# Optimization experiments

Measured on AMD Instinct MI355X. Metric: run time of the kernel, lower is better.

Reference implementation:

```python
import jax, jax.numpy as jnp
import numpy as np

B, CIN, N, K, G, COUT = 8, 128, 2048, 16, 4, 256
NL = COUT // 4          # nl_channels = int(0.25*out_channels) = 64
L = COUT - NL           # l_channels = 192
CL = L // G             # 48 per local head
CNL = NL // G           # 16 per non-local head


def setup_inputs() -> dict:
    key = jax.random.key(0)
    ks = jax.random.split(key, 16)
    s = 0.05
    r = lambda k_, sh: s * jax.random.normal(k_, sh, jnp.float32)
    return {
        "x": jax.random.normal(ks[0], (B, CIN, N, K), jnp.float32),
        "abs_x": jax.random.normal(ks[1], (B, CIN // 2, N, 1), jnp.float32),
        "points": jax.random.normal(ks[2], (B, 3, N), jnp.float32),
        "Wq": r(ks[3], (L, CIN // 2)),
        "Wk": r(ks[4], (L, CIN // 2)),
        "Wv": r(ks[5], (L, CIN)),
        "Wnq": r(ks[6], (NL, CIN // 2)),
        "Wnk": r(ks[7], (NL, CIN // 2)),
        "Wnv1": r(ks[8], (NL, CIN // 2)),
        "Wnv2": r(ks[9], (NL, CIN // 2)),
        "pe_w1": r(ks[10], (3, L)),
        "pe_b1": jnp.zeros((L,), jnp.float32),
        "pe_w2": r(ks[11], (L, L)),
        "pe_b2": jnp.zeros((L,), jnp.float32),
        "npe_w1": r(ks[12], (G, 3, CNL)),
        "npe_b1": jnp.zeros((G, CNL), jnp.float32),
        "npe_w2": r(ks[13], (G, CNL, CNL)),
        "npe_b2": jnp.zeros((G, CNL), jnp.float32),
        "idx": jax.random.randint(ks[14], (B, 1, N, K), 0, N, dtype=jnp.int32),
    }


def _forward(x, abs_x, points, Wq, Wk, Wv, Wnq, Wnk, Wnv1, Wnv2,
             pe_w1, pe_b1, pe_w2, pe_b2, npe_w1, npe_b1, npe_w2, npe_b2, idx):
    b, c, n, k = x.shape
    half = c // 2
    idx_sq = idx[:, 0]                                   # (b,n,k)

    # ---- 1. Local attention over kNN neighbors ----
    lq = jnp.einsum('oc,bcns->bons', Wq, abs_x).reshape(b, G, CL, n, 1)
    lk = jnp.einsum('oc,bcnk->bonk', Wk, x[:, half:] + x[:, :half]).reshape(b, G, CL, n, k)
    lv = jnp.einsum('oc,bcnk->bonk', Wv, x).reshape(b, G, CL, n, k)

    # absolute positional encoding (select_neighbors -> carte MLP)
    nbr = jax.vmap(lambda p, i: p[:, i])(points, idx_sq)  # (b,3,n,k)
    rel = nbr - nbr[..., 0:1]                             # subtract first neighbor
    h = jax.nn.relu(jnp.einsum('bcnk,cd->bnkd', rel, pe_w1) + pe_b1)
    pe = (jnp.einsum('bnkd,de->bnke', h, pe_w2) + pe_b2).transpose(0, 3, 1, 2)
    lk = lk + pe.reshape(b, G, CL, n, k)

    att = jax.nn.softmax((lq * lk).sum(2), axis=-1)       # (b,G,n,k)
    local_feature = jnp.einsum('bgnk,bgcnk->bgcn', att, lv).reshape(b, L, n, 1)

    # ---- scatter-based sparse attention centrality + top-k node selection ----
    idx_flat = idx_sq.reshape(b, n * k)
    att_flat = att.reshape(b, G, n * k)

    def scat(a_g, i):  # a_g: (G, n*k), i: (n*k,)
        return jax.vmap(lambda a: jnp.zeros((n,), a.dtype).at[i].add(a))(a_g)

    cent = jax.vmap(scat)(att_flat, idx_flat)             # (b,G,n)
    vals, inds = jax.lax.top_k(cent, k)                   # (b,G,k)

    # ---- 2. Non-local MHA over selected nodes ----
    a2 = abs_x[..., 0]                                    # (b,half,n)
    nq = jnp.einsum('oc,bcn->bon', Wnq, a2).reshape(b, G, CNL, n)
    nk_ = jnp.einsum('oc,bcn->bon', Wnk, a2).reshape(b, G, CNL, n)
    nv1 = jnp.einsum('oc,bcn->bon', Wnv1, a2).reshape(b, G, CNL, n)
    nv2 = jnp.einsum('oc,bcn->bon', Wnv2, a2).reshape(b, G, CNL, n)

    gi = inds[:, :, None, :]                              # (b,G,1,k)
    nk_sel = jnp.take_along_axis(nk_, gi, axis=3)         # (b,G,CNL,k)
    nv2j = jnp.take_along_axis(nv2, gi, axis=3)           # (b,G,CNL,k)

    # per-group non-local positional encoding (constant over n by construction)
    sel = jnp.take_along_axis(jnp.broadcast_to(points[:, None], (b, G, 3, n)), gi, axis=3)  # (b,G,3,k)
    rel_nl = sel - sel[..., 0:1]
    h2 = jax.nn.relu(jnp.einsum('bgck,gcd->bgkd', rel_nl, npe_w1) + npe_b1[None, :, None, :])
    pe_nl = (jnp.einsum('bgkd,gde->bgke', h2, npe_w2) + npe_b2[None, :, None, :]).transpose(0, 1, 3, 2)  # (b,G,CNL,k)

    att_nl = jax.nn.softmax(jnp.einsum('bgcn,bgck->bgnk', nq, nk_sel + pe_nl), axis=-1)
    # value[b,g,c,n,k] = nv1[...,n] - nv2[...,n] + nv2j[...,k], gated by tanh(centrality)
    w = att_nl * jnp.tanh(vals)[:, :, None, :]            # (b,G,n,k)
    s = w.sum(-1)                                         # (b,G,n)
    nl_feature = (nv1 - nv2) * s[:, :, None, :] + jnp.einsum('bgnk,bgck->bgcn', w, nv2j)
    nl_feature = nl_feature.reshape(b, NL, n, 1)

    return jnp.concatenate([local_feature, nl_feature], axis=1)  # (b,COUT,n,1)


def reference(x, abs_x, points, Wq, Wk, Wv, Wnq, Wnk, Wnv1, Wnv2,
              pe_w1, pe_b1, pe_w2, pe_b2, npe_w1, npe_b1, npe_w2, npe_b2, idx):
    return _forward(x, abs_x, points, Wq, Wk, Wv, Wnq, Wnk, Wnv1, Wnv2,
                    pe_w1, pe_b1, pe_w2, pe_b2, npe_w1, npe_b1, npe_w2, npe_b2, idx)
```

## Files before the change

kernel.cpp:

```cpp
#include <hip/hip_runtime.h>
#include <cstddef>

constexpr int NN = 2048;
constexpr int GG = 4;

__global__ __launch_bounds__(256) void prep_q(const float* __restrict__ Wq,
                                              const float* __restrict__ Wk,
                                              const float* __restrict__ pe_w2,
                                              float* __restrict__ Qbuf) {
    const int g = blockIdx.x >> 6, c2 = blockIdx.x & 63;
    const int row = threadIdx.x;
    float acc = 0.f;
    if (row < 64) {
        for (int j = 0; j < 48; ++j) {
            const int o = g * 48 + j;
            acc = fmaf(Wk[o * 64 + row], Wq[o * 64 + c2], acc);
        }
    } else {
        const int d = row - 64;
        for (int j = 0; j < 48; ++j) {
            const int o = g * 48 + j;
            acc = fmaf(pe_w2[(size_t)d * 192 + o], Wq[o * 64 + c2], acc);
        }
    }
    Qbuf[((size_t)(g * 64 + c2) << 8) + row] = acc;
}

__global__ __launch_bounds__(256, 3) void local_v4(
    const float* __restrict__ x, const float* __restrict__ abs_x,
    const float* __restrict__ points, const float* __restrict__ Wv,
    const float* __restrict__ pe_w1, const float* __restrict__ pe_b1,
    const int* __restrict__ idx, const float* __restrict__ Qbuf,
    float* __restrict__ out, float* __restrict__ cent)
{
    const int bn = blockIdx.x;
    const int b  = bn >> 8;
    const int n0 = (bn & 255) << 3;
    const int tid = threadIdx.x;

    __shared__ int   sidx[128];
    __shared__ float sa2[64][8];
    __shared__ float spts[3][8][16];
    __shared__ float sq[4][8][65];
    __shared__ __align__(16) float s_union[4 * 8 * 193];
    __shared__ float spartA[128][9];
    __shared__ float spartB[128][9];
    __shared__ float satt[4][128];

    float* sw  = s_union;
    float* sxw = s_union;

    if (tid < 128) sidx[tid] = idx[((size_t)b * NN + n0) * 16 + tid];
    for (int i = tid; i < 512; i += 256) {
        int c = i >> 3, nl = i & 7;
        sa2[c][nl] = abs_x[((size_t)b * 64 + c) * NN + n0 + nl];
    }
    __syncthreads();

    for (int i = tid; i < 384; i += 256) {
        int c = i >> 7, r = i & 127;
        spts[c][r >> 4][r & 15] = points[((size_t)b * 3 + c) * NN + sidx[r]];
    }
    for (int g = 0; g < 4; ++g) {
        const float* qb = Qbuf + ((size_t)g << 14) + tid;
        float acc[8] = {0.f, 0.f, 0.f, 0.f, 0.f, 0.f, 0.f, 0.f};
        for (int c2 = 0; c2 < 64; ++c2) {
            const float qv = qb[c2 << 8];
            const float4 a0 = *(const float4*)&sa2[c2][0];
            const float4 a1 = *(const float4*)&sa2[c2][4];
            acc[0] = fmaf(qv, a0.x, acc[0]); acc[1] = fmaf(qv, a0.y, acc[1]);
            acc[2] = fmaf(qv, a0.z, acc[2]); acc[3] = fmaf(qv, a0.w, acc[3]);
            acc[4] = fmaf(qv, a1.x, acc[4]); acc[5] = fmaf(qv, a1.y, acc[5]);
            acc[6] = fmaf(qv, a1.z, acc[6]); acc[7] = fmaf(qv, a1.w, acc[7]);
        }
        if (tid < 64) {
            #pragma unroll
            for (int nl = 0; nl < 8; ++nl) sq[g][nl][tid] = acc[nl];
        } else {
            #pragma unroll
            for (int nl = 0; nl < 8; ++nl) sw[((g << 3) + nl) * 193 + (tid - 64)] = acc[nl];
        }
    }
    __syncthreads();

    {
        const int col = tid & 127, ch = tid >> 7;
        const int nl = col >> 4, kk = col & 15;
        const float* xp = x + (((size_t)(b * 128 + ch * 32) * NN) + n0 + nl) * 16 + kk;
        const float* q0 = &sq[0][nl][ch * 32];
        const float* q1 = &sq[1][nl][ch * 32];
        const float* q2 = &sq[2][nl][ch * 32];
        const float* q3 = &sq[3][nl][ch * 32];
        float a0 = 0.f, a1 = 0.f, a2 = 0.f, a3 = 0.f;
        for (int i = 0; i < 32; ++i) {
            const float xs = xp[0] + xp[(size_t)64 * NN * 16];
            xp += NN * 16;
            a0 = fmaf(q0[i], xs, a0);
            a1 = fmaf(q1[i], xs, a1);
            a2 = fmaf(q2[i], xs, a2);
            a3 = fmaf(q3[i], xs, a3);
        }
        spartA[col][ch * 4 + 0] = a0; spartA[col][ch * 4 + 1] = a1;
        spartA[col][ch * 4 + 2] = a2; spartA[col][ch * 4 + 3] = a3;
    }
    {
        const int col = tid & 127, dh = tid >> 7;
        const int nl = col >> 4, kk = col & 15;
        const float r0 = spts[0][nl][kk] - spts[0][nl][0];
        const float r1 = spts[1][nl][kk] - spts[1][nl][0];
        const float r2 = spts[2][nl][kk] - spts[2][nl][0];
        float p0 = 0.f, p1 = 0.f, p2 = 0.f, p3 = 0.f;
        const int d0 = dh * 96;
        const float* w0 = &sw[((0 << 3) + nl) * 193];
        const float* w1 = &sw[((1 << 3) + nl) * 193];
        const float* w2 = &sw[((2 << 3) + nl) * 193];
        const float* w3 = &sw[((3 << 3) + nl) * 193];
        for (int d = d0; d < d0 + 96; ++d) {
            float h = fmaf(r0, pe_w1[d], fmaf(r1, pe_w1[192 + d], fmaf(r2, pe_w1[384 + d], pe_b1[d])));
            h = fmaxf(h, 0.f);
            p0 = fmaf(h, w0[d], p0);
            p1 = fmaf(h, w1[d], p1);
            p2 = fmaf(h, w2[d], p2);
            p3 = fmaf(h, w3[d], p3);
        }
        spartB[col][dh * 4 + 0] = p0; spartB[col][dh * 4 + 1] = p1;
        spartB[col][dh * 4 + 2] = p2; spartB[col][dh * 4 + 3] = p3;
    }
    __syncthreads();

    if (tid < 32) {
        const int g = tid >> 3, nl = tid & 7;
        float lg[16], m = -1e30f;
        #pragma unroll
        for (int kk = 0; kk < 16; ++kk) {
            const int col = nl * 16 + kk;
            lg[kk] = (spartA[col][g] + spartA[col][4 + g])
                   + (spartB[col][g] + spartB[col][4 + g]);
            m = fmaxf(m, lg[kk]);
        }
        float s = 0.f;
        #pragma unroll
        for (int kk = 0; kk < 16; ++kk) { lg[kk] = __expf(lg[kk] - m); s += lg[kk]; }
        const float inv = 1.f / s;
        #pragma unroll
        for (int kk = 0; kk < 16; ++kk) {
            const float a = lg[kk] * inv;
            satt[g][nl * 16 + kk] = a;
            atomicAdd(&cent[((size_t)(b * GG + g) << 11) + sidx[nl * 16 + kk]], a);
        }
    }
    __syncthreads();

    #pragma unroll
    for (int t = 0; t < 4; ++t) {
        const int i2 = t * 256 + tid;
        const int c = i2 >> 3, nl = i2 & 7;
        const float* xp = x + (((size_t)(b * 128 + c) * NN) + n0 + nl) * 16;
        const float4 x0 = *(const float4*)(xp);
        const float4 x1 = *(const float4*)(xp + 4);
        const float4 x2 = *(const float4*)(xp + 8);
        const float4 x3 = *(const float4*)(xp + 12);
        const float xv[16] = {x0.x, x0.y, x0.z, x0.w, x1.x, x1.y, x1.z, x1.w,
                              x2.x, x2.y, x2.z, x2.w, x3.x, x3.y, x3.z, x3.w};
        #pragma unroll
        for (int g = 0; g < 4; ++g) {
            float v = 0.f;
            #pragma unroll
            for (int kk = 0; kk < 16; ++kk) v = fmaf(xv[kk], satt[g][nl * 16 + kk], v);
            sxw[((g << 7) + c) * 8 + nl] = v;
        }
    }
    __syncthreads();

    for (int i = tid; i < 1536; i += 256) {
        const int o = i >> 3, nl = i & 7;
        const int g = o / 48;
        const float* wv = Wv + (size_t)o * 128;
        const float* xwp = &sxw[(size_t)(g << 7) * 8 + nl];
        float a = 0.f;
        for (int c = 0; c < 128; c += 4) {
            const float4 w4 = *(const float4*)(wv + c);
            a = fmaf(w4.x, xwp[(c + 0) * 8], a);
            a = fmaf(w4.y, xwp[(c + 1) * 8], a);
            a = fmaf(w4.z, xwp[(c + 2) * 8], a);
            a = fmaf(w4.w, xwp[(c + 3) * 8], a);
        }
        out[(((size_t)b << 8) + o) * NN + n0 + nl] = a;
    }
}

__global__ __launch_bounds__(256) void topk_prep_kernel(
    const float* __restrict__ abs_x, const float* __restrict__ points,
    const float* __restrict__ Wnk, const float* __restrict__ Wnv2,
    const float* __restrict__ npe_w1, const float* __restrict__ npe_b1,
    const float* __restrict__ npe_w2, const float* __restrict__ npe_b2,
    const float* __restrict__ cent,
    float* __restrict__ nkpe, float* __restrict__ nv2j, float* __restrict__ tanhv)
{
    const int bg  = blockIdx.x;
    const int b   = bg >> 2, g = bg & 3;
    const int tid = threadIdx.x;
    __shared__ float sc[2048];
    __shared__ float rv[4];  __shared__ int ri[4];
    __shared__ float svals[16]; __shared__ int sinds[16];
    __shared__ float srel[3][16];
    __shared__ float sh2[16][16];

    for (int i = tid; i < 2048; i += 256) sc[i] = cent[((size_t)bg << 11) + i];
    __syncthreads();
    for (int t = 0; t < 16; ++t) {
        float bv = -1e30f; int bi = 1 << 30;
        for (int i = tid; i < 2048; i += 256) {
            float v = sc[i];
            if (v > bv) { bv = v; bi = i; }
        }
        #pragma unroll
        for (int off = 1; off < 64; off <<= 1) {
            float ov = __shfl_xor(bv, off, 64);
            int   oi = __shfl_xor(bi, off, 64);
            if (ov > bv || (ov == bv && oi < bi)) { bv = ov; bi = oi; }
        }
        if ((tid & 63) == 0) { rv[tid >> 6] = bv; ri[tid >> 6] = bi; }
        __syncthreads();
        if (tid == 0) {
            for (int w = 1; w < 4; ++w)
                if (rv[w] > bv || (rv[w] == bv && ri[w] < bi)) { bv = rv[w]; bi = ri[w]; }
            svals[t] = bv; sinds[t] = bi;
            sc[bi] = -1e30f;
        }
        __syncthreads();
    }

    if (tid < 48) {
        int c = tid >> 4, j = tid & 15;
        srel[c][j] = points[((size_t)b * 3 + c) * NN + sinds[j]]
                   - points[((size_t)b * 3 + c) * NN + sinds[0]];
    }
    __syncthreads();
    {
        int j = tid >> 4, d = tid & 15;
        float a = npe_b1[g * 16 + d];
        #pragma unroll
        for (int c = 0; c < 3; ++c) a = fmaf(srel[c][j], npe_w1[((g * 3 + c) << 4) + d], a);
        sh2[j][d] = fmaxf(a, 0.f);
    }
    __syncthreads();
    {
        int c = tid >> 4, j = tid & 15;
        float a = npe_b2[g * 16 + c];
        #pragma unroll
        for (int d = 0; d < 16; ++d) a = fmaf(sh2[j][d], npe_w2[((g * 16 + d) << 4) + c], a);
        float nk = 0.f, nv = 0.f;
        const int col = sinds[j];
        const float* a2  = abs_x + (size_t)b * 64 * NN + col;
        const float* wkr = Wnk  + ((size_t)(g * 16 + c) << 6);
        const float* wvr = Wnv2 + ((size_t)(g * 16 + c) << 6);
        for (int ci = 0; ci < 64; ++ci) {
            float av = a2[(size_t)ci * NN];
            nk = fmaf(wkr[ci], av, nk);
            nv = fmaf(wvr[ci], av, nv);
        }
        nkpe[((size_t)bg << 8) + (c << 4) + j] = nk + a;
        nv2j[((size_t)bg << 8) + (c << 4) + j] = nv;
    }
    if (tid < 16) tanhv[(bg << 4) + tid] = tanhf(svals[tid]);
}

__global__ __launch_bounds__(256) void nonlocal_kernel(
    const float* __restrict__ abs_x,
    const float* __restrict__ Wnq, const float* __restrict__ Wnv1, const float* __restrict__ Wnv2,
    const float* __restrict__ nkpe, const float* __restrict__ nv2j, const float* __restrict__ tanhv,
    float* __restrict__ out)
{
    const int blk = blockIdx.x;
    const int b   = blk >> 5;
    const int n0  = (blk & 31) << 6;
    const int tid = threadIdx.x;
    const int nl  = tid & 63;
    const int g   = tid >> 6;

    __shared__ float sa2[64][64];
    __shared__ float snkpe[4][16][16];
    __shared__ float snv2j[4][16][16];
    __shared__ float stanh[4][16];

    for (int i = tid; i < 64 * 64; i += 256) {
        int ci = i >> 6, c2 = i & 63;
        sa2[ci][c2] = abs_x[((size_t)b * 64 + ci) * NN + n0 + c2];
    }
    for (int i = tid; i < 1024; i += 256) {
        ((float*)snkpe)[i] = nkpe[((size_t)b << 10) + i];
        ((float*)snv2j)[i] = nv2j[((size_t)b << 10) + i];
    }
    if (tid < 64) ((float*)stanh)[tid] = tanhv[(b << 6) + tid];
    __syncthreads();

    float nq[16], nv1[16], nv2[16];
    #pragma unroll
    for (int c = 0; c < 16; ++c) { nq[c] = 0.f; nv1[c] = 0.f; nv2[c] = 0.f; }
    const float* wq  = Wnq  + (size_t)(g << 4) * 64;
    const float* wv1 = Wnv1 + (size_t)(g << 4) * 64;
    const float* wv2 = Wnv2 + (size_t)(g << 4) * 64;
    for (int ci = 0; ci < 64; ++ci) {
        const float a = sa2[ci][nl];
        #pragma unroll
        for (int c = 0; c < 16; ++c) {
            nq[c]  = fmaf(wq [(c << 6) + ci], a, nq[c]);
            nv1[c] = fmaf(wv1[(c << 6) + ci], a, nv1[c]);
            nv2[c] = fmaf(wv2[(c << 6) + ci], a, nv2[c]);
        }
    }

    float lg[16];
    #pragma unroll
    for (int j = 0; j < 16; ++j) {
        float a = 0.f;
        #pragma unroll
        for (int c = 0; c < 16; ++c) a = fmaf(nq[c], snkpe[g][c][j], a);
        lg[j] = a;
    }
    float m = lg[0];
    #pragma unroll
    for (int j = 1; j < 16; ++j) m = fmaxf(m, lg[j]);
    float s = 0.f;
    float w[16];
    #pragma unroll
    for (int j = 0; j < 16; ++j) { w[j] = __expf(lg[j] - m); s += w[j]; }
    const float inv = 1.f / s;
    float ws = 0.f;
    #pragma unroll
    for (int j = 0; j < 16; ++j) { w[j] = w[j] * inv * stanh[g][j]; ws += w[j]; }
    #pragma unroll
    for (int c = 0; c < 16; ++c) {
        float v = (nv1[c] - nv2[c]) * ws;
        #pragma unroll
        for (int j = 0; j < 16; ++j) v = fmaf(w[j], snv2j[g][c][j], v);
        out[(((size_t)b << 8) + 192 + (g << 4) + c) * NN + n0 + nl] = v;
    }
}

extern "C" void kernel_launch(void* const* d_in, const int* in_sizes, int n_in,
                              void* d_out, int out_size, void* d_ws, size_t ws_size,
                              hipStream_t stream)
{
    (void)in_sizes; (void)n_in; (void)out_size; (void)ws_size;
    const float* x      = (const float*)d_in[0];
    const float* abs_x  = (const float*)d_in[1];
    const float* points = (const float*)d_in[2];
    const float* Wq     = (const float*)d_in[3];
    const float* Wk     = (const float*)d_in[4];
    const float* Wv     = (const float*)d_in[5];
    const float* Wnq    = (const float*)d_in[6];
    const float* Wnk    = (const float*)d_in[7];
    const float* Wnv1   = (const float*)d_in[8];
    const float* Wnv2   = (const float*)d_in[9];
    const float* pe_w1  = (const float*)d_in[10];
    const float* pe_b1  = (const float*)d_in[11];
    const float* pe_w2  = (const float*)d_in[12];
    const float* npe_w1 = (const float*)d_in[14];
    const float* npe_b1 = (const float*)d_in[15];
    const float* npe_w2 = (const float*)d_in[16];
    const float* npe_b2 = (const float*)d_in[17];
    const int*   idx    = (const int*)d_in[18];
    float* out = (float*)d_out;

    float* cent  = (float*)d_ws;
    float* Qbuf  = cent + 65536;
    float* nkpeW = Qbuf + 65536;
    float* nv2jW = nkpeW + 8192;
    float* tanhW = nv2jW + 8192;

    hipMemsetAsync(cent, 0, (size_t)65536 * sizeof(float), stream);
    prep_q<<<256, 256, 0, stream>>>(Wq, Wk, pe_w2, Qbuf);
    local_v4<<<2048, 256, 0, stream>>>(x, abs_x, points, Wv, pe_w1, pe_b1,
                                       idx, Qbuf, out, cent);
    topk_prep_kernel<<<32, 256, 0, stream>>>(abs_x, points, Wnk, Wnv2,
                                             npe_w1, npe_b1, npe_w2, npe_b2,
                                             cent, nkpeW, nv2jW, tanhW);
    nonlocal_kernel<<<8 * 32, 256, 0, stream>>>(abs_x, Wnq, Wnv1, Wnv2,
                                                nkpeW, nv2jW, tanhW, out);
}
```

Baseline: 235.0 us.

## Halve points per block in local kernel and prefetch x before softmax

The local attention kernel now handles 4 points per block instead of 8. That doubles the grid to 4096 blocks, shrinks shared memory, and raises the launch-bounds occupancy hint from 3 to 4 blocks. The logit reductions are split four ways across channel and d ranges instead of two. The x tile used in the weighted sum is loaded into registers before the softmax so its latency overlaps the softmax phase. Costs include recomputing Q/W projections per block twice as often, more register pressure from holding 32 prefetched values, and less reuse of Wv loads per block.

```diff
diff --git a/kernel.cpp b/kernel.cpp
--- a/kernel.cpp
+++ b/kernel.cpp
@@ -26,7 +26,7 @@
     Qbuf[((size_t)(g * 64 + c2) << 8) + row] = acc;
 }
 
-__global__ __launch_bounds__(256, 3) void local_v4(
+__global__ __launch_bounds__(256, 4) void local_v5(
     const float* __restrict__ x, const float* __restrict__ abs_x,
     const float* __restrict__ points, const float* __restrict__ Wv,
     const float* __restrict__ pe_w1, const float* __restrict__ pe_b1,
@@ -34,88 +34,90 @@
     float* __restrict__ out, float* __restrict__ cent)
 {
     const int bn = blockIdx.x;
-    const int b  = bn >> 8;
-    const int n0 = (bn & 255) << 3;
+    const int b  = bn >> 9;
+    const int n0 = (bn & 511) << 2;
     const int tid = threadIdx.x;
 
-    __shared__ int   sidx[128];
-    __shared__ float sa2[64][8];
-    __shared__ float spts[3][8][16];
-    __shared__ float sq[4][8][65];
-    __shared__ __align__(16) float s_union[4 * 8 * 193];
-    __shared__ float spartA[128][9];
-    __shared__ float spartB[128][9];
-    __shared__ float satt[4][128];
+    __shared__ int   sidx[64];
+    __shared__ float sa2[64][4];
+    __shared__ float spts[3][4][16];
+    __shared__ float sq[4][4][65];
+    __shared__ __align__(16) float s_union[3104];
+    __shared__ float spartA[64][17];
+    __shared__ float spartB[64][17];
+    __shared__ float satt[4][64];
 
     float* sw  = s_union;
     float* sxw = s_union;
 
-    if (tid < 128) sidx[tid] = idx[((size_t)b * NN + n0) * 16 + tid];
-    for (int i = tid; i < 512; i += 256) {
-        int c = i >> 3, nl = i & 7;
+    if (tid < 64) sidx[tid] = idx[((size_t)b * NN + n0) * 16 + tid];
+    if (tid < 256) {
+        int c = tid >> 2, nl = tid & 3;
         sa2[c][nl] = abs_x[((size_t)b * 64 + c) * NN + n0 + nl];
     }
     __syncthreads();
 
-    for (int i = tid; i < 384; i += 256) {
-        int c = i >> 7, r = i & 127;
+    if (tid < 192) {
+        int c = tid >> 6, r = tid & 63;
         spts[c][r >> 4][r & 15] = points[((size_t)b * 3 + c) * NN + sidx[r]];
     }
+    #pragma unroll
     for (int g = 0; g < 4; ++g) {
         const float* qb = Qbuf + ((size_t)g << 14) + tid;
-        float acc[8] = {0.f, 0.f, 0.f, 0.f, 0.f, 0.f, 0.f, 0.f};
+        float a0 = 0.f, a1 = 0.f, a2v = 0.f, a3 = 0.f;
         for (int c2 = 0; c2 < 64; ++c2) {
             const float qv = qb[c2 << 8];
-            const float4 a0 = *(const float4*)&sa2[c2][0];
-            const float4 a1 = *(const float4*)&sa2[c2][4];
-            acc[0] = fmaf(qv, a0.x, acc[0]); acc[1] = fmaf(qv, a0.y, acc[1]);
-            acc[2] = fmaf(qv, a0.z, acc[2]); acc[3] = fmaf(qv, a0.w, acc[3]);
-            acc[4] = fmaf(qv, a1.x, acc[4]); acc[5] = fmaf(qv, a1.y, acc[5]);
-            acc[6] = fmaf(qv, a1.z, acc[6]); acc[7] = fmaf(qv, a1.w, acc[7]);
+            const float4 av = *(const float4*)&sa2[c2][0];
+            a0 = fmaf(qv, av.x, a0); a1 = fmaf(qv, av.y, a1);
+            a2v = fmaf(qv, av.z, a2v); a3 = fmaf(qv, av.w, a3);
         }
         if (tid < 64) {
-            #pragma unroll
-            for (int nl = 0; nl < 8; ++nl) sq[g][nl][tid] = acc[nl];
+            sq[g][0][tid] = a0; sq[g][1][tid] = a1;
+            sq[g][2][tid] = a2v; sq[g][3][tid] = a3;
         } else {
-            #pragma unroll
-            for (int nl = 0; nl < 8; ++nl) sw[((g << 3) + nl) * 193 + (tid - 64)] = acc[nl];
+            const int d = tid - 64;
+            sw[((g << 2) + 0) * 193 + d] = a0;
+            sw[((g << 2) + 1) * 193 + d] = a1;
+            sw[((g << 2) + 2) * 193 + d] = a2v;
+            sw[((g << 2) + 3) * 193 + d] = a3;
         }
     }
     __syncthreads();
 
     {
-        const int col = tid & 127, ch = tid >> 7;
+        const int col = tid & 63, ch = tid >> 6;
         const int nl = col >> 4, kk = col & 15;
-        const float* xp = x + (((size_t)(b * 128 + ch * 32) * NN) + n0 + nl) * 16 + kk;
-        const float* q0 = &sq[0][nl][ch * 32];
-        const float* q1 = &sq[1][nl][ch * 32];
-        const float* q2 = &sq[2][nl][ch * 32];
-        const float* q3 = &sq[3][nl][ch * 32];
-        float a0 = 0.f, a1 = 0.f, a2 = 0.f, a3 = 0.f;
-        for (int i = 0; i < 32; ++i) {
+        const float* xp = x + (((size_t)(b * 128 + ch * 16) * NN) + n0 + nl) * 16 + kk;
+        const float* q0 = &sq[0][nl][ch * 16];
+        const float* q1 = &sq[1][nl][ch * 16];
+        const float* q2 = &sq[2][nl][ch * 16];
+        const float* q3 = &sq[3][nl][ch * 16];
+        float a0 = 0.f, a1 = 0.f, a2v = 0.f, a3 = 0.f;
+        #pragma unroll 4
+        for (int i = 0; i < 16; ++i) {
             const float xs = xp[0] + xp[(size_t)64 * NN * 16];
             xp += NN * 16;
             a0 = fmaf(q0[i], xs, a0);
             a1 = fmaf(q1[i], xs, a1);
-            a2 = fmaf(q2[i], xs, a2);
+            a2v = fmaf(q2[i], xs, a2v);
             a3 = fmaf(q3[i], xs, a3);
         }
         spartA[col][ch * 4 + 0] = a0; spartA[col][ch * 4 + 1] = a1;
-        spartA[col][ch * 4 + 2] = a2; spartA[col][ch * 4 + 3] = a3;
+        spartA[col][ch * 4 + 2] = a2v; spartA[col][ch * 4 + 3] = a3;
     }
     {
-        const int col = tid & 127, dh = tid >> 7;
+        const int col = tid & 63, dh = tid >> 6;
         const int nl = col >> 4, kk = col & 15;
         const float r0 = spts[0][nl][kk] - spts[0][nl][0];
         const float r1 = spts[1][nl][kk] - spts[1][nl][0];
         const float r2 = spts[2][nl][kk] - spts[2][nl][0];
         float p0 = 0.f, p1 = 0.f, p2 = 0.f, p3 = 0.f;
-        const int d0 = dh * 96;
-        const float* w0 = &sw[((0 << 3) + nl) * 193];
-        const float* w1 = &sw[((1 << 3) + nl) * 193];
-        const float* w2 = &sw[((2 << 3) + nl) * 193];
-        const float* w3 = &sw[((3 << 3) + nl) * 193];
-        for (int d = d0; d < d0 + 96; ++d) {
+        const int d0 = dh * 48;
+        const float* w0 = &sw[((0 << 2) + nl) * 193];
+        const float* w1 = &sw[((1 << 2) + nl) * 193];
+        const float* w2 = &sw[((2 << 2) + nl) * 193];
+        const float* w3 = &sw[((3 << 2) + nl) * 193];
+        for (int d = d0; d < d0 + 48; ++d) {
             float h = fmaf(r0, pe_w1[d], fmaf(r1, pe_w1[192 + d], fmaf(r2, pe_w1[384 + d], pe_b1[d])));
             h = fmaxf(h, 0.f);
             p0 = fmaf(h, w0[d], p0);
@@ -128,14 +130,26 @@
     }
     __syncthreads();
 
-    if (tid < 32) {
-        const int g = tid >> 3, nl = tid & 7;
+    float xv[2][16];
+    #pragma unroll
+    for (int t = 0; t < 2; ++t) {
+        const int i2 = t * 256 + tid;
+        const int c = i2 >> 2, nl = i2 & 3;
+        const float* xp = x + (((size_t)(b * 128 + c) * NN) + n0 + nl) * 16;
+        *(float4*)&xv[t][0]  = *(const float4*)(xp);
+        *(float4*)&xv[t][4]  = *(const float4*)(xp + 4);
+        *(float4*)&xv[t][8]  = *(const float4*)(xp + 8);
+        *(float4*)&xv[t][12] = *(const float4*)(xp + 12);
+    }
+
+    if (tid < 16) {
+        const int g = tid >> 2, nl = tid & 3;
         float lg[16], m = -1e30f;
         #pragma unroll
         for (int kk = 0; kk < 16; ++kk) {
             const int col = nl * 16 + kk;
-            lg[kk] = (spartA[col][g] + spartA[col][4 + g])
-                   + (spartB[col][g] + spartB[col][4 + g]);
+            lg[kk] = (spartA[col][g] + spartA[col][4 + g] + spartA[col][8 + g] + spartA[col][12 + g])
+                   + (spartB[col][g] + spartB[col][4 + g] + spartB[col][8 + g] + spartB[col][12 + g]);
             m = fmaxf(m, lg[kk]);
         }
         float s = 0.f;
@@ -152,38 +166,33 @@
     __syncthreads();
 
     #pragma unroll
-    for (int t = 0; t < 4; ++t) {
+    for (int t = 0; t < 2; ++t) {
         const int i2 = t * 256 + tid;
-        const int c = i2 >> 3, nl = i2 & 7;
-        const float* xp = x + (((size_t)(b * 128 + c) * NN) + n0 + nl) * 16;
-        const float4 x0 = *(const float4*)(xp);
-        const float4 x1 = *(const float4*)(xp + 4);
-        const float4 x2 = *(const float4*)(xp + 8);
-        const float4 x3 = *(const float4*)(xp + 12);
-        const float xv[16] = {x0.x, x0.y, x0.z, x0.w, x1.x, x1.y, x1.z, x1.w,
-                              x2.x, x2.y, x2.z, x2.w, x3.x, x3.y, x3.z, x3.w};
+        const int c = i2 >> 2, nl = i2 & 3;
         #pragma unroll
         for (int g = 0; g < 4; ++g) {
             float v = 0.f;
             #pragma unroll
-            for (int kk = 0; kk < 16; ++kk) v = fmaf(xv[kk], satt[g][nl * 16 + kk], v);
-            sxw[((g << 7) + c) * 8 + nl] = v;
-        }
-    }
-    __syncthreads();
-
-    for (int i = tid; i < 1536; i += 256) {
-        const int o = i >> 3, nl = i & 7;
+            for (int kk = 0; kk < 16; ++kk) v = fmaf(xv[t][kk], satt[g][nl * 16 + kk], v);
+            sxw[(((g << 7) + c) << 2) + nl] = v;
+        }
+    }
+    __syncthreads();
+
+    #pragma unroll
+    for (int rep = 0; rep < 3; ++rep) {
+        const int i = rep * 256 + tid;
+        const int o = i >> 2, nl = i & 3;
         const int g = o / 48;
         const float* wv = Wv + (size_t)o * 128;
-        const float* xwp = &sxw[(size_t)(g << 7) * 8 + nl];
+        const float* xwp = &sxw[((size_t)(g << 7) << 2) + nl];
         float a = 0.f;
         for (int c = 0; c < 128; c += 4) {
             const float4 w4 = *(const float4*)(wv + c);
-            a = fmaf(w4.x, xwp[(c + 0) * 8], a);
-            a = fmaf(w4.y, xwp[(c + 1) * 8], a);
-            a = fmaf(w4.z, xwp[(c + 2) * 8], a);
-            a = fmaf(w4.w, xwp[(c + 3) * 8], a);
+            a = fmaf(w4.x, xwp[(c + 0) << 2], a);
+            a = fmaf(w4.y, xwp[(c + 1) << 2], a);
+            a = fmaf(w4.z, xwp[(c + 2) << 2], a);
+            a = fmaf(w4.w, xwp[(c + 3) << 2], a);
         }
         out[(((size_t)b << 8) + o) * NN + n0 + nl] = a;
     }
@@ -372,7 +381,7 @@
 
     hipMemsetAsync(cent, 0, (size_t)65536 * sizeof(float), stream);
     prep_q<<<256, 256, 0, stream>>>(Wq, Wk, pe_w2, Qbuf);
-    local_v4<<<2048, 256, 0, stream>>>(x, abs_x, points, Wv, pe_w1, pe_b1,
+    local_v5<<<4096, 256, 0, stream>>>(x, abs_x, points, Wv, pe_w1, pe_b1,
                                        idx, Qbuf, out, cent);
     topk_prep_kernel<<<32, 256, 0, stream>>>(abs_x, points, Wnk, Wnv2,
                                              npe_w1, npe_b1, npe_w2, npe_b2,
```

After: 248.6 us. +5.8%, slower.

## Shrink local kernel shared memory and raise occupancy; widen topk block

Applied to the files above, without the earlier changes.

Restructures the local attention kernel to cut shared memory: the q-projection and positional-weight buffers now share one aliased region, the positional-encoding weights are computed two groups at a time in two passes, and the two partial-logit arrays are merged into one accumulated array. Launch bounds rise from 3 to 6 blocks per CU. The Wv projection and attention-weighted sum switch to contiguous float4 shared reads, and the centrality atomics move to the end of the kernel. The topk kernel now uses 512 threads per block. The extra passes add barriers and recompute work, traded for more resident waves to hide global load latency.

```diff
diff --git a/kernel.cpp b/kernel.cpp
--- a/kernel.cpp
+++ b/kernel.cpp
@@ -26,7 +26,7 @@
     Qbuf[((size_t)(g * 64 + c2) << 8) + row] = acc;
 }
 
-__global__ __launch_bounds__(256, 3) void local_v4(
+__global__ __launch_bounds__(256, 6) void local_v7(
     const float* __restrict__ x, const float* __restrict__ abs_x,
     const float* __restrict__ points, const float* __restrict__ Wv,
     const float* __restrict__ pe_w1, const float* __restrict__ pe_b1,
@@ -40,15 +40,15 @@
 
     __shared__ int   sidx[128];
     __shared__ float sa2[64][8];
-    __shared__ float spts[3][8][16];
-    __shared__ float sq[4][8][65];
-    __shared__ __align__(16) float s_union[4 * 8 * 193];
-    __shared__ float spartA[128][9];
-    __shared__ float spartB[128][9];
-    __shared__ float satt[4][128];
-
-    float* sw  = s_union;
-    float* sxw = s_union;
+    __shared__ __align__(16) float s_big[4224];
+    __shared__ float spart[128][9];
+    __shared__ float s_small[544];
+
+    float* sq   = s_big;
+    float* sw2  = s_big;
+    float* sxw  = s_big;
+    float* spts = s_small;
+    float* satt = s_small;
 
     if (tid < 128) sidx[tid] = idx[((size_t)b * NN + n0) * 16 + tid];
     for (int i = tid; i < 512; i += 256) {
@@ -58,84 +58,122 @@
     __syncthreads();
 
     for (int i = tid; i < 384; i += 256) {
-        int c = i >> 7, r = i & 127;
-        spts[c][r >> 4][r & 15] = points[((size_t)b * 3 + c) * NN + sidx[r]];
-    }
-    for (int g = 0; g < 4; ++g) {
-        const float* qb = Qbuf + ((size_t)g << 14) + tid;
-        float acc[8] = {0.f, 0.f, 0.f, 0.f, 0.f, 0.f, 0.f, 0.f};
+        int c3 = i >> 7, r = i & 127;
+        spts[(c3 * 8 + (r >> 4)) * 16 + (r & 15)] =
+            points[((size_t)b * 3 + c3) * NN + sidx[r]];
+    }
+    {
+        const int g = tid >> 6, row = tid & 63;
+        const float* qb = Qbuf + (((size_t)g * 64) << 8) + row;
+        float a0 = 0.f, a1 = 0.f, a2v = 0.f, a3 = 0.f,
+              a4 = 0.f, a5 = 0.f, a6 = 0.f, a7 = 0.f;
         for (int c2 = 0; c2 < 64; ++c2) {
             const float qv = qb[c2 << 8];
-            const float4 a0 = *(const float4*)&sa2[c2][0];
-            const float4 a1 = *(const float4*)&sa2[c2][4];
-            acc[0] = fmaf(qv, a0.x, acc[0]); acc[1] = fmaf(qv, a0.y, acc[1]);
-            acc[2] = fmaf(qv, a0.z, acc[2]); acc[3] = fmaf(qv, a0.w, acc[3]);
-            acc[4] = fmaf(qv, a1.x, acc[4]); acc[5] = fmaf(qv, a1.y, acc[5]);
-            acc[6] = fmaf(qv, a1.z, acc[6]); acc[7] = fmaf(qv, a1.w, acc[7]);
-        }
-        if (tid < 64) {
-            #pragma unroll
-            for (int nl = 0; nl < 8; ++nl) sq[g][nl][tid] = acc[nl];
-        } else {
-            #pragma unroll
-            for (int nl = 0; nl < 8; ++nl) sw[((g << 3) + nl) * 193 + (tid - 64)] = acc[nl];
-        }
-    }
-    __syncthreads();
+            const float4 v0 = *(const float4*)&sa2[c2][0];
+            const float4 v1 = *(const float4*)&sa2[c2][4];
+            a0 = fmaf(qv, v0.x, a0); a1 = fmaf(qv, v0.y, a1);
+            a2v = fmaf(qv, v0.z, a2v); a3 = fmaf(qv, v0.w, a3);
+            a4 = fmaf(qv, v1.x, a4); a5 = fmaf(qv, v1.y, a5);
+            a6 = fmaf(qv, v1.z, a6); a7 = fmaf(qv, v1.w, a7);
+        }
+        const int base = (g << 3) * 65 + row;
+        sq[base + 0 * 65] = a0; sq[base + 1 * 65] = a1;
+        sq[base + 2 * 65] = a2v; sq[base + 3 * 65] = a3;
+        sq[base + 4 * 65] = a4; sq[base + 5 * 65] = a5;
+        sq[base + 6 * 65] = a6; sq[base + 7 * 65] = a7;
+    }
+    __syncthreads();
+
+    const int col = tid & 127, dh = tid >> 7;
+    const int nlc = col >> 4, kkc = col & 15;
 
     {
-        const int col = tid & 127, ch = tid >> 7;
-        const int nl = col >> 4, kk = col & 15;
-        const float* xp = x + (((size_t)(b * 128 + ch * 32) * NN) + n0 + nl) * 16 + kk;
-        const float* q0 = &sq[0][nl][ch * 32];
-        const float* q1 = &sq[1][nl][ch * 32];
-        const float* q2 = &sq[2][nl][ch * 32];
-        const float* q3 = &sq[3][nl][ch * 32];
-        float a0 = 0.f, a1 = 0.f, a2 = 0.f, a3 = 0.f;
+        const float* xp = x + (((size_t)(b * 128 + dh * 32) * NN) + n0 + nlc) * 16 + kkc;
+        const float* q0 = &sq[((0 << 3) + nlc) * 65 + dh * 32];
+        const float* q1 = &sq[((1 << 3) + nlc) * 65 + dh * 32];
+        const float* q2 = &sq[((2 << 3) + nlc) * 65 + dh * 32];
+        const float* q3 = &sq[((3 << 3) + nlc) * 65 + dh * 32];
+        float a0 = 0.f, a1 = 0.f, a2v = 0.f, a3 = 0.f;
         for (int i = 0; i < 32; ++i) {
             const float xs = xp[0] + xp[(size_t)64 * NN * 16];
             xp += NN * 16;
             a0 = fmaf(q0[i], xs, a0);
             a1 = fmaf(q1[i], xs, a1);
-            a2 = fmaf(q2[i], xs, a2);
+            a2v = fmaf(q2[i], xs, a2v);
             a3 = fmaf(q3[i], xs, a3);
         }
-        spartA[col][ch * 4 + 0] = a0; spartA[col][ch * 4 + 1] = a1;
-        spartA[col][ch * 4 + 2] = a2; spartA[col][ch * 4 + 3] = a3;
-    }
-    {
-        const int col = tid & 127, dh = tid >> 7;
-        const int nl = col >> 4, kk = col & 15;
-        const float r0 = spts[0][nl][kk] - spts[0][nl][0];
-        const float r1 = spts[1][nl][kk] - spts[1][nl][0];
-        const float r2 = spts[2][nl][kk] - spts[2][nl][0];
-        float p0 = 0.f, p1 = 0.f, p2 = 0.f, p3 = 0.f;
-        const int d0 = dh * 96;
-        const float* w0 = &sw[((0 << 3) + nl) * 193];
-        const float* w1 = &sw[((1 << 3) + nl) * 193];
-        const float* w2 = &sw[((2 << 3) + nl) * 193];
-        const float* w3 = &sw[((3 << 3) + nl) * 193];
-        for (int d = d0; d < d0 + 96; ++d) {
-            float h = fmaf(r0, pe_w1[d], fmaf(r1, pe_w1[192 + d], fmaf(r2, pe_w1[384 + d], pe_b1[d])));
-            h = fmaxf(h, 0.f);
-            p0 = fmaf(h, w0[d], p0);
-            p1 = fmaf(h, w1[d], p1);
-            p2 = fmaf(h, w2[d], p2);
-            p3 = fmaf(h, w3[d], p3);
-        }
-        spartB[col][dh * 4 + 0] = p0; spartB[col][dh * 4 + 1] = p1;
-        spartB[col][dh * 4 + 2] = p2; spartB[col][dh * 4 + 3] = p3;
-    }
-    __syncthreads();
+        spart[col][dh * 4 + 0] = a0; spart[col][dh * 4 + 1] = a1;
+        spart[col][dh * 4 + 2] = a2v; spart[col][dh * 4 + 3] = a3;
+    }
+    __syncthreads();
+
+    const float r0 = spts[(0 * 8 + nlc) * 16 + kkc] - spts[(0 * 8 + nlc) * 16];
+    const float r1 = spts[(1 * 8 + nlc) * 16 + kkc] - spts[(1 * 8 + nlc) * 16];
+    const float r2 = spts[(2 * 8 + nlc) * 16 + kkc] - spts[(2 * 8 + nlc) * 16];
+    #pragma unroll
+    for (int p = 0; p < 2; ++p) {
+        if (tid < 192) {
+            const int d = tid;
+            float w00=0.f,w01=0.f,w02=0.f,w03=0.f,w04=0.f,w05=0.f,w06=0.f,w07=0.f;
+            float w10=0.f,w11=0.f,w12=0.f,w13=0.f,w14=0.f,w15=0.f,w16=0.f,w17=0.f;
+            const float* qb0 = Qbuf + (((size_t)(2 * p + 0) * 64) << 8) + 64 + d;
+            const float* qb1 = Qbuf + (((size_t)(2 * p + 1) * 64) << 8) + 64 + d;
+            for (int c2 = 0; c2 < 64; ++c2) {
+                const float qv0 = qb0[c2 << 8];
+                const float qv1 = qb1[c2 << 8];
+                const float4 v0 = *(const float4*)&sa2[c2][0];
+                const float4 v1 = *(const float4*)&sa2[c2][4];
+                w00 = fmaf(qv0, v0.x, w00); w01 = fmaf(qv0, v0.y, w01);
+                w02 = fmaf(qv0, v0.z, w02); w03 = fmaf(qv0, v0.w, w03);
+                w04 = fmaf(qv0, v1.x, w04); w05 = fmaf(qv0, v1.y, w05);
+                w06 = fmaf(qv0, v1.z, w06); w07 = fmaf(qv0, v1.w, w07);
+                w10 = fmaf(qv1, v0.x, w10); w11 = fmaf(qv1, v0.y, w11);
+                w12 = fmaf(qv1, v0.z, w12); w13 = fmaf(qv1, v0.w, w13);
+                w14 = fmaf(qv1, v1.x, w14); w15 = fmaf(qv1, v1.y, w15);
+                w16 = fmaf(qv1, v1.z, w16); w17 = fmaf(qv1, v1.w, w17);
+            }
+            sw2[(0 * 8 + 0) * 196 + d] = w00; sw2[(0 * 8 + 1) * 196 + d] = w01;
+            sw2[(0 * 8 + 2) * 196 + d] = w02; sw2[(0 * 8 + 3) * 196 + d] = w03;
+            sw2[(0 * 8 + 4) * 196 + d] = w04; sw2[(0 * 8 + 5) * 196 + d] = w05;
+            sw2[(0 * 8 + 6) * 196 + d] = w06; sw2[(0 * 8 + 7) * 196 + d] = w07;
+            sw2[(1 * 8 + 0) * 196 + d] = w10; sw2[(1 * 8 + 1) * 196 + d] = w11;
+            sw2[(1 * 8 + 2) * 196 + d] = w12; sw2[(1 * 8 + 3) * 196 + d] = w13;
+            sw2[(1 * 8 + 4) * 196 + d] = w14; sw2[(1 * 8 + 5) * 196 + d] = w15;
+            sw2[(1 * 8 + 6) * 196 + d] = w16; sw2[(1 * 8 + 7) * 196 + d] = w17;
+        }
+        __syncthreads();
+        {
+            float pB0 = 0.f, pB1 = 0.f;
+            const float* w0 = &sw2[(0 * 8 + nlc) * 196];
+            const float* w1 = &sw2[(1 * 8 + nlc) * 196];
+            const int d0 = dh * 96;
+            for (int d = d0; d < d0 + 96; d += 4) {
+                const float4 w1a = *(const float4*)&pe_w1[d];
+                const float4 w1b = *(const float4*)&pe_w1[192 + d];
+                const float4 w1c = *(const float4*)&pe_w1[384 + d];
+                const float4 bb  = *(const float4*)&pe_b1[d];
+                const float h0 = fmaxf(fmaf(r0, w1a.x, fmaf(r1, w1b.x, fmaf(r2, w1c.x, bb.x))), 0.f);
+                const float h1 = fmaxf(fmaf(r0, w1a.y, fmaf(r1, w1b.y, fmaf(r2, w1c.y, bb.y))), 0.f);
+                const float h2 = fmaxf(fmaf(r0, w1a.z, fmaf(r1, w1b.z, fmaf(r2, w1c.z, bb.z))), 0.f);
+                const float h3 = fmaxf(fmaf(r0, w1a.w, fmaf(r1, w1b.w, fmaf(r2, w1c.w, bb.w))), 0.f);
+                const float4 wa = *(const float4*)&w0[d];
+                const float4 wb = *(const float4*)&w1[d];
+                pB0 = fmaf(h0, wa.x, fmaf(h1, wa.y, fmaf(h2, wa.z, fmaf(h3, wa.w, pB0))));
+                pB1 = fmaf(h0, wb.x, fmaf(h1, wb.y, fmaf(h2, wb.z, fmaf(h3, wb.w, pB1))));
+            }
+            spart[col][dh * 4 + 2 * p + 0] += pB0;
+            spart[col][dh * 4 + 2 * p + 1] += pB1;
+        }
+        __syncthreads();
+    }
 
     if (tid < 32) {
         const int g = tid >> 3, nl = tid & 7;
         float lg[16], m = -1e30f;
         #pragma unroll
         for (int kk = 0; kk < 16; ++kk) {
-            const int col = nl * 16 + kk;
-            lg[kk] = (spartA[col][g] + spartA[col][4 + g])
-                   + (spartB[col][g] + spartB[col][4 + g]);
+            const int cc = nl * 16 + kk;
+            lg[kk] = spart[cc][g] + spart[cc][4 + g];
             m = fmaxf(m, lg[kk]);
         }
         float s = 0.f;
@@ -143,11 +181,7 @@
         for (int kk = 0; kk < 16; ++kk) { lg[kk] = __expf(lg[kk] - m); s += lg[kk]; }
         const float inv = 1.f / s;
         #pragma unroll
-        for (int kk = 0; kk < 16; ++kk) {
-            const float a = lg[kk] * inv;
-            satt[g][nl * 16 + kk] = a;
-            atomicAdd(&cent[((size_t)(b * GG + g) << 11) + sidx[nl * 16 + kk]], a);
-        }
+        for (int kk = 0; kk < 16; ++kk) satt[nl * 68 + g * 16 + kk] = lg[kk] * inv;
     }
     __syncthreads();
 
@@ -160,36 +194,50 @@
         const float4 x1 = *(const float4*)(xp + 4);
         const float4 x2 = *(const float4*)(xp + 8);
         const float4 x3 = *(const float4*)(xp + 12);
-        const float xv[16] = {x0.x, x0.y, x0.z, x0.w, x1.x, x1.y, x1.z, x1.w,
-                              x2.x, x2.y, x2.z, x2.w, x3.x, x3.y, x3.z, x3.w};
+        const float* at = &satt[nl * 68];
         #pragma unroll
         for (int g = 0; g < 4; ++g) {
+            const float* a = at + g * 16;
             float v = 0.f;
-            #pragma unroll
-            for (int kk = 0; kk < 16; ++kk) v = fmaf(xv[kk], satt[g][nl * 16 + kk], v);
-            sxw[((g << 7) + c) * 8 + nl] = v;
-        }
-    }
-    __syncthreads();
-
-    for (int i = tid; i < 1536; i += 256) {
+            v = fmaf(x0.x, a[0],  v); v = fmaf(x0.y, a[1],  v);
+            v = fmaf(x0.z, a[2],  v); v = fmaf(x0.w, a[3],  v);
+            v = fmaf(x1.x, a[4],  v); v = fmaf(x1.y, a[5],  v);
+            v = fmaf(x1.z, a[6],  v); v = fmaf(x1.w, a[7],  v);
+            v = fmaf(x2.x, a[8],  v); v = fmaf(x2.y, a[9],  v);
+            v = fmaf(x2.z, a[10], v); v = fmaf(x2.w, a[11], v);
+            v = fmaf(x3.x, a[12], v); v = fmaf(x3.y, a[13], v);
+            v = fmaf(x3.z, a[14], v); v = fmaf(x3.w, a[15], v);
+            sxw[((g << 3) + nl) * 132 + c] = v;
+        }
+    }
+    __syncthreads();
+
+    #pragma unroll
+    for (int rep = 0; rep < 6; ++rep) {
+        const int i = rep * 256 + tid;
         const int o = i >> 3, nl = i & 7;
         const int g = o / 48;
-        const float* wv = Wv + (size_t)o * 128;
-        const float* xwp = &sxw[(size_t)(g << 7) * 8 + nl];
+        const float* wv  = Wv + (size_t)o * 128;
+        const float* xwp = &sxw[((g << 3) + nl) * 132];
         float a = 0.f;
         for (int c = 0; c < 128; c += 4) {
-            const float4 w4 = *(const float4*)(wv + c);
-            a = fmaf(w4.x, xwp[(c + 0) * 8], a);
-            a = fmaf(w4.y, xwp[(c + 1) * 8], a);
-            a = fmaf(w4.z, xwp[(c + 2) * 8], a);
-            a = fmaf(w4.w, xwp[(c + 3) * 8], a);
+            const float4 w4  = *(const float4*)(wv + c);
+            const float4 xw4 = *(const float4*)(xwp + c);
+            a = fmaf(w4.x, xw4.x, fmaf(w4.y, xw4.y, fmaf(w4.z, xw4.z, fmaf(w4.w, xw4.w, a))));
         }
         out[(((size_t)b << 8) + o) * NN + n0 + nl] = a;
     }
+
+    if (tid < 32) {
+        const int g = tid >> 3, nl = tid & 7;
+        #pragma unroll
+        for (int kk = 0; kk < 16; ++kk)
+            atomicAdd(&cent[((size_t)(b * GG + g) << 11) + sidx[nl * 16 + kk]],
+                      satt[nl * 68 + g * 16 + kk]);
+    }
 }
 
-__global__ __launch_bounds__(256) void topk_prep_kernel(
+__global__ __launch_bounds__(512) void topk_prep_kernel(
     const float* __restrict__ abs_x, const float* __restrict__ points,
     const float* __restrict__ Wnk, const float* __restrict__ Wnv2,
     const float* __restrict__ npe_w1, const float* __restrict__ npe_b1,
@@ -201,16 +249,16 @@
     const int b   = bg >> 2, g = bg & 3;
     const int tid = threadIdx.x;
     __shared__ float sc[2048];
-    __shared__ float rv[4];  __shared__ int ri[4];
+    __shared__ float rv[8];  __shared__ int ri[8];
     __shared__ float svals[16]; __shared__ int sinds[16];
     __shared__ float srel[3][16];
     __shared__ float sh2[16][16];
 
-    for (int i = tid; i < 2048; i += 256) sc[i] = cent[((size_t)bg << 11) + i];
+    for (int i = tid; i < 2048; i += 512) sc[i] = cent[((size_t)bg << 11) + i];
     __syncthreads();
     for (int t = 0; t < 16; ++t) {
         float bv = -1e30f; int bi = 1 << 30;
-        for (int i = tid; i < 2048; i += 256) {
+        for (int i = tid; i < 2048; i += 512) {
             float v = sc[i];
             if (v > bv) { bv = v; bi = i; }
         }
@@ -223,7 +271,7 @@
         if ((tid & 63) == 0) { rv[tid >> 6] = bv; ri[tid >> 6] = bi; }
         __syncthreads();
         if (tid == 0) {
-            for (int w = 1; w < 4; ++w)
+            for (int w = 1; w < 8; ++w)
                 if (rv[w] > bv || (rv[w] == bv && ri[w] < bi)) { bv = rv[w]; bi = ri[w]; }
             svals[t] = bv; sinds[t] = bi;
             sc[bi] = -1e30f;
@@ -237,7 +285,7 @@
                    - points[((size_t)b * 3 + c) * NN + sinds[0]];
     }
     __syncthreads();
-    {
+    if (tid < 256) {
         int j = tid >> 4, d = tid & 15;
         float a = npe_b1[g * 16 + d];
         #pragma unroll
@@ -245,14 +293,14 @@
         sh2[j][d] = fmaxf(a, 0.f);
     }
     __syncthreads();
-    {
+    if (tid < 256) {
         int c = tid >> 4, j = tid & 15;
         float a = npe_b2[g * 16 + c];
         #pragma unroll
         for (int d = 0; d < 16; ++d) a = fmaf(sh2[j][d], npe_w2[((g * 16 + d) << 4) + c], a);
         float nk = 0.f, nv = 0.f;
-        const int col = sinds[j];
-        const float* a2  = abs_x + (size_t)b * 64 * NN + col;
+        const int colj = sinds[j];
+        const float* a2  = abs_x + (size_t)b * 64 * NN + colj;
         const float* wkr = Wnk  + ((size_t)(g * 16 + c) << 6);
         const float* wvr = Wnv2 + ((size_t)(g * 16 + c) << 6);
         for (int ci = 0; ci < 64; ++ci) {
@@ -372,9 +420,9 @@
 
     hipMemsetAsync(cent, 0, (size_t)65536 * sizeof(float), stream);
     prep_q<<<256, 256, 0, stream>>>(Wq, Wk, pe_w2, Qbuf);
-    local_v4<<<2048, 256, 0, stream>>>(x, abs_x, points, Wv, pe_w1, pe_b1,
+    local_v7<<<2048, 256, 0, stream>>>(x, abs_x, points, Wv, pe_w1, pe_b1,
                                        idx, Qbuf, out, cent);
-    topk_prep_kernel<<<32, 256, 0, stream>>>(abs_x, points, Wnk, Wnv2,
+    topk_prep_kernel<<<32, 512, 0, stream>>>(abs_x, points, Wnk, Wnv2,
                                              npe_w1, npe_b1, npe_w2, npe_b2,
                                              cent, nkpeW, nv2jW, tanhW);
     nonlocal_kernel<<<8 * 32, 256, 0, stream>>>(abs_x, Wnq, Wnv1, Wnv2,
```

After: 293.3 us. +24.8%, slower.
